# Optimization experiments

Measured on AMD Instinct MI355X. Metric: run time of the kernel, lower is better.

Reference implementation:

```python
import jax, jax.numpy as jnp
import numpy as np
import math

NUM_HEADS = 32
KV_CHANNELS = 128
LAYER_NUMBER = 4
# apply_query_key_layer_scaling=True: norm_factor = sqrt(head_dim) * layer_number,
# then scores are re-multiplied by layer_number in fp32 (numerics trick).
NORM_FACTOR = math.sqrt(KV_CHANNELS) * LAYER_NUMBER
COEFF = float(LAYER_NUMBER)
NEG = -1e9


def setup_inputs() -> dict:
    key = jax.random.key(0)
    k1, k2, k3 = jax.random.split(key, 3)
    b, h, s, d = 2, NUM_HEADS, 2048, KV_CHANNELS
    q = jax.random.normal(k1, (b, h, s, d), dtype=jnp.float32)
    k = jax.random.normal(k2, (b, h, s, d), dtype=jnp.float32)
    v = jax.random.normal(k3, (b, h, s, d), dtype=jnp.float32)
    # additive causal mask: 0 where allowed (j <= i), large negative where masked
    causal = jnp.tril(jnp.ones((s, s), dtype=bool))
    mask = jnp.where(causal, 0.0, NEG).astype(jnp.float32)[None, None, :, :]
    mask = jnp.broadcast_to(mask, (b, 1, s, s))
    return {"query_layer": q, "key_layer": k, "value_layer": v, "attention_mask": mask}


def reference(query_layer, key_layer, value_layer, attention_mask):
    b, h, sq, d = query_layer.shape
    skv = key_layer.shape[2]
    # baddbmm with beta=0, alpha=1/norm_factor  ==  (Q K^T) / norm_factor
    scores = jnp.einsum('bhqd,bhkd->bhqk', query_layer, key_layer) / NORM_FACTOR
    # attention_softmax_in_fp32 + layer scaling coefficient
    scores = scores.astype(jnp.float32) * COEFF
    scores = scores + attention_mask[:, :, :, :skv]
    probs = jax.nn.softmax(scores, axis=-1).astype(value_layer.dtype)
    # dropout p=0.0 -> identity
    context = jnp.einsum('bhqk,bhkd->bhqd', probs, value_layer)
    # transpose to [b, sq, h, d] then merge heads -> [b, sq, h*d]
    context = context.transpose(0, 2, 1, 3).reshape(b, sq, h * d)
    return context
```

## Files before the change

### kernel.cpp

```cpp
#include <hip/hip_runtime.h>
#include <cstdint>
#include <cstddef>

typedef __attribute__((ext_vector_type(8))) __bf16 bf16x8;
typedef __attribute__((ext_vector_type(4))) __bf16 bf16x4;
typedef __attribute__((ext_vector_type(4))) short s16x4;
typedef __attribute__((ext_vector_type(4))) float f32x4;
typedef __attribute__((ext_vector_type(2))) float f32x2;

#define SEQ 2048
#define DIM 128
#define NHEAD 32
#define NBATCH 2
#define NHEADS_TOTAL (NHEAD * NBATCH)
#define QSC (0.08838834764831845f * 1.4426950408889634f)

#define KV_TILE 32
#define TILES_PER_HEAD (SEQ / KV_TILE)
#define TILE_ELEMS (KV_TILE * DIM)
#define K_WS_BYTES ((size_t)NHEADS_TOTAL * TILES_PER_HEAD * TILE_ELEMS * 2)
#define WS_NEEDED (2 * K_WS_BYTES)

#define PS 40

__device__ __forceinline__ float fexp2(float x) {
#if __has_builtin(__builtin_amdgcn_exp2f)
  return __builtin_amdgcn_exp2f(x);
#else
  return __expf(x * 0.69314718055994531f);
#endif
}

__device__ __forceinline__ f32x4 mfma16(bf16x4 a, bf16x4 b, f32x4 c) {
#if __has_builtin(__builtin_amdgcn_mfma_f32_16x16x16_bf16)
  return __builtin_amdgcn_mfma_f32_16x16x16_bf16(a, b, c, 0, 0, 0);
#else
  return __builtin_amdgcn_mfma_f32_16x16x16bf16_1k(
      __builtin_bit_cast(s16x4, a), __builtin_bit_cast(s16x4, b), c, 0, 0, 0);
#endif
}

__device__ __forceinline__ void tile_barrier() {
  __builtin_amdgcn_sched_barrier(0);
  asm volatile("s_waitcnt lgkmcnt(0)" ::: "memory");
  __builtin_amdgcn_sched_barrier(0);
  __builtin_amdgcn_s_barrier();
  __builtin_amdgcn_sched_barrier(0);
}

__global__ __launch_bounds__(256) void glm_prepass(const float* __restrict__ Kg,
                                                   const float* __restrict__ Vg,
                                                   __bf16* __restrict__ Kws,
                                                   __bf16* __restrict__ Vws) {
  __shared__ float Vl[32 * 132];
  const int hd = blockIdx.x >> 6;
  const int t  = blockIdx.x & 63;
  const int i  = threadIdx.x;
  const int kv = i >> 3, seg = i & 7;
  const size_t src   = ((size_t)hd * SEQ + (size_t)t * 32 + kv) * DIM + seg * 16;
  const size_t tbase = (size_t)(hd * TILES_PER_HEAD + t) * TILE_ELEMS;

  {
    f32x4 a = *(const f32x4*)(Kg + src);
    f32x4 b = *(const f32x4*)(Kg + src + 4);
    f32x4 c4 = *(const f32x4*)(Kg + src + 8);
    f32x4 d4 = *(const f32x4*)(Kg + src + 12);
    bf16x8 A, B;
#pragma unroll
    for (int j = 0; j < 4; ++j) {
      A[j] = (__bf16)a[j]; A[4 + j] = (__bf16)b[j];
      B[j] = (__bf16)c4[j]; B[4 + j] = (__bf16)d4[j];
    }
    const int cf = kv >> 4, lc = kv & 15, cc = seg >> 1, q0 = (seg & 1) * 2;
    const int chunkA = (cf * 4 + cc) * 64 + q0 * 16 + lc;
    *(bf16x8*)&Kws[tbase + (size_t)chunkA * 8] = A;
    *(bf16x8*)&Kws[tbase + (size_t)(chunkA + 16) * 8] = B;
  }

  {
    f32x4 a = *(const f32x4*)(Vg + src);
    f32x4 b = *(const f32x4*)(Vg + src + 4);
    f32x4 c4 = *(const f32x4*)(Vg + src + 8);
    f32x4 d4 = *(const f32x4*)(Vg + src + 12);
    float* vl = &Vl[kv * 132 + seg * 16];
    *(f32x4*)(vl + 0) = a; *(f32x4*)(vl + 4) = b;
    *(f32x4*)(vl + 8) = c4; *(f32x4*)(vl + 12) = d4;
  }
  __syncthreads();
#pragma unroll
  for (int u = 0; u < 2; ++u) {
    const int ch = i * 2 + u;
    const int nt = ch >> 6, kvg = (ch >> 4) & 3, dd = ch & 15;
    bf16x8 wv;
#pragma unroll
    for (int e = 0; e < 8; ++e) wv[e] = (__bf16)Vl[(kvg * 8 + e) * 132 + nt * 16 + dd];
    *(bf16x8*)&Vws[tbase + (size_t)ch * 8] = wv;
  }
}

__global__ __launch_bounds__(256, 3) void glm_attn_main(const float* __restrict__ Qg,
                                                        const __bf16* __restrict__ Kws,
                                                        const __bf16* __restrict__ Vws,
                                                        float* __restrict__ Out) {
  __shared__ __align__(16) __bf16 Kb[2][TILE_ELEMS];
  __shared__ __align__(16) __bf16 Vb[2][TILE_ELEMS];

  const int tid  = threadIdx.x;
  const int w    = tid >> 6;
  const int lane = tid & 63;
  const int quad = lane >> 4;
  const int lcol = lane & 15;

  const int lin  = (int)blockIdx.x + ((int)blockIdx.y << 3) + ((int)blockIdx.z << 8);
  const int xcd  = lin & 7;
  const int k    = lin >> 3;
  const int head = xcd + ((k >> 3) << 3);
  const int pair = k & 7;
  const int hi   = head & 31, bi = head >> 5;
  const int hd   = bi * NHEAD + hi;

  const float*  Qh   = Qg + (size_t)hd * SEQ * DIM;
  const __bf16* Ksrc = Kws + (size_t)hd * TILES_PER_HEAD * TILE_ELEMS;
  const __bf16* Vsrc = Vws + (size_t)hd * TILES_PER_HEAD * TILE_ELEMS;

  bf16x8 kst0, kst1, vst0, vst1;

#define PREFETCH_REGS(tt)                                                   \
  {                                                                         \
    const __bf16* ks = Ksrc + (size_t)(tt) * TILE_ELEMS + (size_t)tid * 8;  \
    const __bf16* vs = Vsrc + (size_t)(tt) * TILE_ELEMS + (size_t)tid * 8;  \
    kst0 = *(const bf16x8*)ks;    kst1 = *(const bf16x8*)(ks + 2048);       \
    vst0 = *(const bf16x8*)vs;    vst1 = *(const bf16x8*)(vs + 2048);       \
  }

#define WRITE_LDS(b)                                                        \
  {                                                                         \
    *(bf16x8*)&Kb[b][tid * 8]        = kst0;                                \
    *(bf16x8*)&Kb[b][tid * 8 + 2048] = kst1;                                \
    *(bf16x8*)&Vb[b][tid * 8]        = vst0;                                \
    *(bf16x8*)&Vb[b][tid * 8 + 2048] = vst1;                                \
  }

  const int vofs0 = ((quad >> 1)) * 128 + lcol * 8 + (quad & 1) * 4;
  const int vofs1 = (2 + (quad >> 1)) * 128 + lcol * 8 + (quad & 1) * 4;

  for (int band = 0; band < 2; ++band) {
    const int qx = band ? (15 - pair) : pair;
    const int qb = qx * 128;
    const int T = qx * 4 + 4;
    const int Tfull = qx * 4;

    PREFETCH_REGS(0);

    bf16x8 qf[2][4];
#pragma unroll
    for (int m = 0; m < 2; ++m) {
      const float* qp = Qh + (size_t)(qb + w * 32 + m * 16 + lcol) * DIM + quad * 8;
#pragma unroll
      for (int cc = 0; cc < 4; ++cc) {
        f32x4 a = *(const f32x4*)(qp + cc * 32);
        f32x4 b = *(const f32x4*)(qp + cc * 32 + 4);
        bf16x8 t;
#pragma unroll
        for (int j = 0; j < 4; ++j) {
          t[j] = (__bf16)(a[j] * QSC);
          t[4 + j] = (__bf16)(b[j] * QSC);
        }
        qf[m][cc] = t;
      }
    }

    f32x4 o[2][8];
#pragma unroll
    for (int m = 0; m < 2; ++m)
#pragma unroll
      for (int n = 0; n < 8; ++n) o[m][n] = f32x4{0.f, 0.f, 0.f, 0.f};
    float lsum[2] = {0.0f, 0.0f};

    tile_barrier();
    WRITE_LDS(0);
    PREFETCH_REGS(1);

    for (int t = 0; t < T; ++t) {
      const int cur = t & 1;
      tile_barrier();

      const __bf16* Kc = Kb[cur];
      const __bf16* Vc = Vb[cur];

      f32x4 s2[2][2];
      s2[0][0] = s2[0][1] = s2[1][0] = s2[1][1] = f32x4{0.f, 0.f, 0.f, 0.f};
#pragma unroll
      for (int cc = 0; cc < 4; ++cc) {
        bf16x8 k0 = *(const bf16x8*)&Kc[cc * 512 + lane * 8];
        bf16x8 k1 = *(const bf16x8*)&Kc[(4 + cc) * 512 + lane * 8];
        s2[0][0] = __builtin_amdgcn_mfma_f32_16x16x32_bf16(k0, qf[0][cc], s2[0][0], 0, 0, 0);
        s2[0][1] = __builtin_amdgcn_mfma_f32_16x16x32_bf16(k0, qf[1][cc], s2[0][1], 0, 0, 0);
        s2[1][0] = __builtin_amdgcn_mfma_f32_16x16x32_bf16(k1, qf[0][cc], s2[1][0], 0, 0, 0);
        s2[1][1] = __builtin_amdgcn_mfma_f32_16x16x32_bf16(k1, qf[1][cc], s2[1][1], 0, 0, 0);
      }

      if (t + 1 < T) {
        if (cur) WRITE_LDS(0) else WRITE_LDS(1)
        if (t + 2 < T) PREFETCH_REGS(t + 2);
      }

      bf16x4 pb[2][2];
#pragma unroll
      for (int m = 0; m < 2; ++m) {
        float pv[2][4];
        if (t < Tfull) {
#pragma unroll
          for (int cf = 0; cf < 2; ++cf)
#pragma unroll
            for (int rr = 0; rr < 4; ++rr)
              pv[cf][rr] = fexp2(fminf(s2[cf][m][rr], 30.0f));
        } else {
          const int qg = qb + w * 32 + m * 16 + lcol;
          const int kv0 = t * 32 + quad * 4;
#pragma unroll
          for (int cf = 0; cf < 2; ++cf)
#pragma unroll
            for (int rr = 0; rr < 4; ++rr) {
              const int kvg = kv0 + cf * 16 + rr;
              pv[cf][rr] = (kvg <= qg) ? fexp2(fminf(s2[cf][m][rr], 30.0f)) : 0.0f;
            }
        }
#pragma unroll
        for (int cf = 0; cf < 2; ++cf) {
          lsum[m] += pv[cf][0] + pv[cf][1] + pv[cf][2] + pv[cf][3];
          bf16x4 pc;
#pragma unroll
          for (int rr = 0; rr < 4; ++rr) pc[rr] = (__bf16)pv[cf][rr];
          pb[m][cf] = pc;
        }
      }

#pragma unroll
      for (int nt = 0; nt < 8; ++nt) {
        bf16x4 v0 = *(const bf16x4*)&Vc[nt * 512 + vofs0];
        bf16x4 v1 = *(const bf16x4*)&Vc[nt * 512 + vofs1];
        o[0][nt] = mfma16(v0, pb[0][0], o[0][nt]);
        o[0][nt] = mfma16(v1, pb[0][1], o[0][nt]);
        o[1][nt] = mfma16(v0, pb[1][0], o[1][nt]);
        o[1][nt] = mfma16(v1, pb[1][1], o[1][nt]);
      }
    }

#pragma unroll
    for (int m = 0; m < 2; ++m) {
      float v = lsum[m];
      v += __shfl_xor(v, 16);
      v += __shfl_xor(v, 32);
      const float inv = 1.0f / v;
      const int q = qb + w * 32 + m * 16 + lcol;
      float* op = Out + ((size_t)bi * SEQ + q) * (NHEAD * DIM) + hi * DIM + quad * 4;
#pragma unroll
      for (int nt = 0; nt < 8; ++nt) {
        f32x4 st;
        st[0] = o[m][nt][0] * inv;
        st[1] = o[m][nt][1] * inv;
        st[2] = o[m][nt][2] * inv;
        st[3] = o[m][nt][3] * inv;
        *(f32x4*)(op + nt * 16) = st;
      }
    }
  }
}

__global__ __launch_bounds__(256, 2) void glm_attn_fused(
    const float* __restrict__ Qg, const float* __restrict__ Kg,
    const float* __restrict__ Vg, float* __restrict__ Out) {
  __shared__ __align__(16) __bf16 Kb[32 * DIM];
  __shared__ __align__(16) __bf16 Vb[32 * DIM];
  __shared__ __align__(16) __bf16 Pt[4][32 * PS];

  const int tid  = threadIdx.x;
  const int w    = tid >> 6;
  const int lane = tid & 63;
  const int quad = lane >> 4;
  const int lcol = lane & 15;

  const int qx = (int)gridDim.x - 1 - (int)blockIdx.x;
  const int qb = qx * 128;
  const int hi = blockIdx.y, bi = blockIdx.z;
  const int hd = bi * NHEAD + hi;

  const float* Qh = Qg + (size_t)hd * SEQ * DIM;
  const float* Kh = Kg + (size_t)hd * SEQ * DIM;
  const float* Vh = Vg + (size_t)hd * SEQ * DIM;

  const float* kbase = Kh + (size_t)lcol * DIM + w * 32 + quad * 8;
  const int vnt = tid >> 5, vkvg = (tid >> 3) & 3, vdd = (tid & 7) * 2;
  const float* vbase = Vh + (size_t)(vkvg * 8) * DIM + vnt * 16 + vdd;

  f32x4 kr0, kr1, kr2, kr3;
  f32x2 vr0, vr1, vr2, vr3, vr4, vr5, vr6, vr7;

#define PREFETCH_F(tt)                                                \
  {                                                                   \
    const float* ka = kbase + (size_t)(tt) * (32 * DIM);              \
    kr0 = *(const f32x4*)(ka);                                        \
    kr1 = *(const f32x4*)(ka + 4);                                    \
    kr2 = *(const f32x4*)(ka + 16 * DIM);                             \
    kr3 = *(const f32x4*)(ka + 16 * DIM + 4);                         \
    const float* va = vbase + (size_t)(tt) * (32 * DIM);              \
    vr0 = *(const f32x2*)(va + 0 * DIM);                              \
    vr1 = *(const f32x2*)(va + 1 * DIM);                              \
    vr2 = *(const f32x2*)(va + 2 * DIM);                              \
    vr3 = *(const f32x2*)(va + 3 * DIM);                              \
    vr4 = *(const f32x2*)(va + 4 * DIM);                              \
    vr5 = *(const f32x2*)(va + 5 * DIM);                              \
    vr6 = *(const f32x2*)(va + 6 * DIM);                              \
    vr7 = *(const f32x2*)(va + 7 * DIM);                              \
  }

  PREFETCH_F(0);

  bf16x8 qf[2][4];
#pragma unroll
  for (int m = 0; m < 2; ++m) {
    const float* qp = Qh + (size_t)(qb + w * 32 + m * 16 + lcol) * DIM + quad * 8;
#pragma unroll
    for (int c = 0; c < 4; ++c) {
      f32x4 a = *(const f32x4*)(qp + c * 32);
      f32x4 b = *(const f32x4*)(qp + c * 32 + 4);
      bf16x8 tq;
#pragma unroll
      for (int j = 0; j < 4; ++j) {
        tq[j] = (__bf16)(a[j] * QSC);
        tq[4 + j] = (__bf16)(b[j] * QSC);
      }
      qf[m][c] = tq;
    }
  }

  f32x4 o[2][8];
#pragma unroll
  for (int m = 0; m < 2; ++m)
#pragma unroll
    for (int n = 0; n < 8; ++n) o[m][n] = f32x4{0.f, 0.f, 0.f, 0.f};
  float lsum[2][4];
#pragma unroll
  for (int m = 0; m < 2; ++m)
#pragma unroll
    for (int r = 0; r < 4; ++r) lsum[m][r] = 0.0f;

  const int T = qx * 4 + 4;
  const int Tfull = qx * 4;

  for (int t = 0; t < T; ++t) {
    __syncthreads();
    {
      bf16x8 sA, sB;
#pragma unroll
      for (int j = 0; j < 4; ++j) {
        sA[j] = (__bf16)kr0[j]; sA[4 + j] = (__bf16)kr1[j];
        sB[j] = (__bf16)kr2[j]; sB[4 + j] = (__bf16)kr3[j];
      }
      *(bf16x8*)&Kb[tid * 8]        = sA;
      *(bf16x8*)&Kb[tid * 8 + 2048] = sB;
      bf16x8 v0, v1;
      v0[0] = (__bf16)vr0[0]; v1[0] = (__bf16)vr0[1];
      v0[1] = (__bf16)vr1[0]; v1[1] = (__bf16)vr1[1];
      v0[2] = (__bf16)vr2[0]; v1[2] = (__bf16)vr2[1];
      v0[3] = (__bf16)vr3[0]; v1[3] = (__bf16)vr3[1];
      v0[4] = (__bf16)vr4[0]; v1[4] = (__bf16)vr4[1];
      v0[5] = (__bf16)vr5[0]; v1[5] = (__bf16)vr5[1];
      v0[6] = (__bf16)vr6[0]; v1[6] = (__bf16)vr6[1];
      v0[7] = (__bf16)vr7[0]; v1[7] = (__bf16)vr7[1];
      *(bf16x8*)&Vb[tid * 16]     = v0;
      *(bf16x8*)&Vb[tid * 16 + 8] = v1;
    }
    __syncthreads();
    if (t + 1 < T) PREFETCH_F(t + 1);

    f32x4 s[2][2];
    s[0][0] = s[0][1] = s[1][0] = s[1][1] = f32x4{0.f, 0.f, 0.f, 0.f};
#pragma unroll
    for (int c = 0; c < 4; ++c) {
      bf16x8 k0 = *(const bf16x8*)&Kb[c * 512 + lane * 8];
      bf16x8 k1 = *(const bf16x8*)&Kb[(4 + c) * 512 + lane * 8];
      s[0][0] = __builtin_amdgcn_mfma_f32_16x16x32_bf16(qf[0][c], k0, s[0][0], 0, 0, 0);
      s[1][0] = __builtin_amdgcn_mfma_f32_16x16x32_bf16(qf[1][c], k0, s[1][0], 0, 0, 0);
      s[0][1] = __builtin_amdgcn_mfma_f32_16x16x32_bf16(qf[0][c], k1, s[0][1], 0, 0, 0);
      s[1][1] = __builtin_amdgcn_mfma_f32_16x16x32_bf16(qf[1][c], k1, s[1][1], 0, 0, 0);
    }

    __bf16* pw = Pt[w];
    if (t < Tfull) {
#pragma unroll
      for (int m = 0; m < 2; ++m)
#pragma unroll
        for (int cf = 0; cf < 2; ++cf)
#pragma unroll
          for (int r = 0; r < 4; ++r) {
            const float p = fexp2(fminf(s[m][cf][r], 30.0f));
            lsum[m][r] += p;
            pw[(m * 16 + quad * 4 + r) * PS + cf * 16 + lcol] = (__bf16)p;
          }
    } else {
      const int kvb = t * 32;
#pragma unroll
      for (int m = 0; m < 2; ++m) {
        const int rowb = qb + w * 32 + m * 16 + quad * 4;
#pragma unroll
        for (int cf = 0; cf < 2; ++cf) {
          const int col = kvb + cf * 16 + lcol;
#pragma unroll
          for (int r = 0; r < 4; ++r) {
            const float p = (col <= rowb + r) ? fexp2(fminf(s[m][cf][r], 30.0f)) : 0.0f;
            lsum[m][r] += p;
            pw[(m * 16 + quad * 4 + r) * PS + cf * 16 + lcol] = (__bf16)p;
          }
        }
      }
    }

    bf16x8 pf0 = *(const bf16x8*)&pw[lcol * PS + quad * 8];
    bf16x8 pf1 = *(const bf16x8*)&pw[(16 + lcol) * PS + quad * 8];
#pragma unroll
    for (int nt = 0; nt < 8; ++nt) {
      bf16x8 vf = *(const bf16x8*)&Vb[nt * 512 + lane * 8];
      o[0][nt] = __builtin_amdgcn_mfma_f32_16x16x32_bf16(pf0, vf, o[0][nt], 0, 0, 0);
      o[1][nt] = __builtin_amdgcn_mfma_f32_16x16x32_bf16(pf1, vf, o[1][nt], 0, 0, 0);
    }
  }

#pragma unroll
  for (int m = 0; m < 2; ++m)
#pragma unroll
    for (int r = 0; r < 4; ++r) {
      float v = lsum[m][r];
      v += __shfl_xor(v, 1); v += __shfl_xor(v, 2);
      v += __shfl_xor(v, 4); v += __shfl_xor(v, 8);
      lsum[m][r] = 1.0f / v;
    }
#pragma unroll
  for (int m = 0; m < 2; ++m) {
    const int row0 = qb + w * 32 + m * 16 + quad * 4;
#pragma unroll
    for (int r = 0; r < 4; ++r) {
      const float inv = lsum[m][r];
      float* op = Out + ((size_t)bi * SEQ + row0 + r) * (NHEAD * DIM) + hi * DIM + lcol;
#pragma unroll
      for (int nt = 0; nt < 8; ++nt) op[nt * 16] = o[m][nt][r] * inv;
    }
  }
}

extern "C" void kernel_launch(void* const* d_in, const int* in_sizes, int n_in,
                              void* d_out, int out_size, void* d_ws, size_t ws_size,
                              hipStream_t stream) {
  const float* Q = (const float*)d_in[0];
  const float* K = (const float*)d_in[1];
  const float* V = (const float*)d_in[2];
  float* Out = (float*)d_out;

  if (ws_size >= WS_NEEDED) {
    __bf16* Kws = (__bf16*)d_ws;
    __bf16* Vws = (__bf16*)((char*)d_ws + K_WS_BYTES);
    glm_prepass<<<dim3(NHEADS_TOTAL * TILES_PER_HEAD), 256, 0, stream>>>(K, V, Kws, Vws);
    glm_attn_main<<<dim3(8, NHEAD, NBATCH), 256, 0, stream>>>(Q, Kws, Vws, Out);
  } else {
    glm_attn_fused<<<dim3(SEQ / 128, NHEAD, NBATCH), 256, 0, stream>>>(Q, K, V, Out);
  }
}
```

Baseline: 326.1 us.

## Halve query tile to 64 rows per block and double grid size

Shrinks the main attention kernel's query band from 128 to 64 rows, so each wave handles 16 query rows instead of 32, and doubles the grid to 16x32x2 blocks while still pairing bands for causal load balance. Per-thread accumulators drop by half and launch bounds rise to 4 blocks per CU, aiming for more parallelism and occupancy. The cost is that each K/V tile loaded into LDS now serves half as many queries, which doubles K/V global and LDS traffic per unit of work.

```diff
diff --git a/kernel.cpp b/kernel.cpp
--- a/kernel.cpp
+++ b/kernel.cpp
@@ -98,7 +98,7 @@
   }
 }
 
-__global__ __launch_bounds__(256, 3) void glm_attn_main(const float* __restrict__ Qg,
+__global__ __launch_bounds__(256, 4) void glm_attn_main(const float* __restrict__ Qg,
                                                         const __bf16* __restrict__ Kws,
                                                         const __bf16* __restrict__ Vws,
                                                         float* __restrict__ Out) {
@@ -111,11 +111,11 @@
   const int quad = lane >> 4;
   const int lcol = lane & 15;
 
-  const int lin  = (int)blockIdx.x + ((int)blockIdx.y << 3) + ((int)blockIdx.z << 8);
+  const int lin  = (int)blockIdx.x + ((int)blockIdx.y << 4) + ((int)blockIdx.z << 9);
   const int xcd  = lin & 7;
   const int k    = lin >> 3;
-  const int head = xcd + ((k >> 3) << 3);
-  const int pair = k & 7;
+  const int head = xcd + ((k >> 4) << 3);
+  const int pair = k & 15;
   const int hi   = head & 31, bi = head >> 5;
   const int hd   = bi * NHEAD + hi;
 
@@ -145,17 +145,16 @@
   const int vofs1 = (2 + (quad >> 1)) * 128 + lcol * 8 + (quad & 1) * 4;
 
   for (int band = 0; band < 2; ++band) {
-    const int qx = band ? (15 - pair) : pair;
-    const int qb = qx * 128;
-    const int T = qx * 4 + 4;
-    const int Tfull = qx * 4;
+    const int qx = band ? (31 - pair) : pair;
+    const int qb = qx * 64;
+    const int T = qx * 2 + 2;
+    const int Tfull = qx * 2;
 
     PREFETCH_REGS(0);
 
-    bf16x8 qf[2][4];
-#pragma unroll
-    for (int m = 0; m < 2; ++m) {
-      const float* qp = Qh + (size_t)(qb + w * 32 + m * 16 + lcol) * DIM + quad * 8;
+    bf16x8 qf[4];
+    {
+      const float* qp = Qh + (size_t)(qb + w * 16 + lcol) * DIM + quad * 8;
 #pragma unroll
       for (int cc = 0; cc < 4; ++cc) {
         f32x4 a = *(const f32x4*)(qp + cc * 32);
@@ -166,16 +165,14 @@
           t[j] = (__bf16)(a[j] * QSC);
           t[4 + j] = (__bf16)(b[j] * QSC);
         }
-        qf[m][cc] = t;
-      }
-    }
-
-    f32x4 o[2][8];
-#pragma unroll
-    for (int m = 0; m < 2; ++m)
-#pragma unroll
-      for (int n = 0; n < 8; ++n) o[m][n] = f32x4{0.f, 0.f, 0.f, 0.f};
-    float lsum[2] = {0.0f, 0.0f};
+        qf[cc] = t;
+      }
+    }
+
+    f32x4 o[8];
+#pragma unroll
+    for (int n = 0; n < 8; ++n) o[n] = f32x4{0.f, 0.f, 0.f, 0.f};
+    float lsum = 0.0f;
 
     tile_barrier();
     WRITE_LDS(0);
@@ -188,16 +185,14 @@
       const __bf16* Kc = Kb[cur];
       const __bf16* Vc = Vb[cur];
 
-      f32x4 s2[2][2];
-      s2[0][0] = s2[0][1] = s2[1][0] = s2[1][1] = f32x4{0.f, 0.f, 0.f, 0.f};
+      f32x4 s2[2];
+      s2[0] = s2[1] = f32x4{0.f, 0.f, 0.f, 0.f};
 #pragma unroll
       for (int cc = 0; cc < 4; ++cc) {
         bf16x8 k0 = *(const bf16x8*)&Kc[cc * 512 + lane * 8];
         bf16x8 k1 = *(const bf16x8*)&Kc[(4 + cc) * 512 + lane * 8];
-        s2[0][0] = __builtin_amdgcn_mfma_f32_16x16x32_bf16(k0, qf[0][cc], s2[0][0], 0, 0, 0);
-        s2[0][1] = __builtin_amdgcn_mfma_f32_16x16x32_bf16(k0, qf[1][cc], s2[0][1], 0, 0, 0);
-        s2[1][0] = __builtin_amdgcn_mfma_f32_16x16x32_bf16(k1, qf[0][cc], s2[1][0], 0, 0, 0);
-        s2[1][1] = __builtin_amdgcn_mfma_f32_16x16x32_bf16(k1, qf[1][cc], s2[1][1], 0, 0, 0);
+        s2[0] = __builtin_amdgcn_mfma_f32_16x16x32_bf16(k0, qf[cc], s2[0], 0, 0, 0);
+        s2[1] = __builtin_amdgcn_mfma_f32_16x16x32_bf16(k1, qf[cc], s2[1], 0, 0, 0);
       }
 
       if (t + 1 < T) {
@@ -205,34 +200,33 @@
         if (t + 2 < T) PREFETCH_REGS(t + 2);
       }
 
-      bf16x4 pb[2][2];
-#pragma unroll
-      for (int m = 0; m < 2; ++m) {
+      bf16x4 pb[2];
+      {
         float pv[2][4];
         if (t < Tfull) {
 #pragma unroll
           for (int cf = 0; cf < 2; ++cf)
 #pragma unroll
             for (int rr = 0; rr < 4; ++rr)
-              pv[cf][rr] = fexp2(fminf(s2[cf][m][rr], 30.0f));
+              pv[cf][rr] = fexp2(fminf(s2[cf][rr], 30.0f));
         } else {
-          const int qg = qb + w * 32 + m * 16 + lcol;
+          const int qg = qb + w * 16 + lcol;
           const int kv0 = t * 32 + quad * 4;
 #pragma unroll
           for (int cf = 0; cf < 2; ++cf)
 #pragma unroll
             for (int rr = 0; rr < 4; ++rr) {
               const int kvg = kv0 + cf * 16 + rr;
-              pv[cf][rr] = (kvg <= qg) ? fexp2(fminf(s2[cf][m][rr], 30.0f)) : 0.0f;
+              pv[cf][rr] = (kvg <= qg) ? fexp2(fminf(s2[cf][rr], 30.0f)) : 0.0f;
             }
         }
 #pragma unroll
         for (int cf = 0; cf < 2; ++cf) {
-          lsum[m] += pv[cf][0] + pv[cf][1] + pv[cf][2] + pv[cf][3];
+          lsum += pv[cf][0] + pv[cf][1] + pv[cf][2] + pv[cf][3];
           bf16x4 pc;
 #pragma unroll
           for (int rr = 0; rr < 4; ++rr) pc[rr] = (__bf16)pv[cf][rr];
-          pb[m][cf] = pc;
+          pb[cf] = pc;
         }
       }
 
@@ -240,28 +234,25 @@
       for (int nt = 0; nt < 8; ++nt) {
         bf16x4 v0 = *(const bf16x4*)&Vc[nt * 512 + vofs0];
         bf16x4 v1 = *(const bf16x4*)&Vc[nt * 512 + vofs1];
-        o[0][nt] = mfma16(v0, pb[0][0], o[0][nt]);
-        o[0][nt] = mfma16(v1, pb[0][1], o[0][nt]);
-        o[1][nt] = mfma16(v0, pb[1][0], o[1][nt]);
-        o[1][nt] = mfma16(v1, pb[1][1], o[1][nt]);
-      }
-    }
-
-#pragma unroll
-    for (int m = 0; m < 2; ++m) {
-      float v = lsum[m];
+        o[nt] = mfma16(v0, pb[0], o[nt]);
+        o[nt] = mfma16(v1, pb[1], o[nt]);
+      }
+    }
+
+    {
+      float v = lsum;
       v += __shfl_xor(v, 16);
       v += __shfl_xor(v, 32);
       const float inv = 1.0f / v;
-      const int q = qb + w * 32 + m * 16 + lcol;
+      const int q = qb + w * 16 + lcol;
       float* op = Out + ((size_t)bi * SEQ + q) * (NHEAD * DIM) + hi * DIM + quad * 4;
 #pragma unroll
       for (int nt = 0; nt < 8; ++nt) {
         f32x4 st;
-        st[0] = o[m][nt][0] * inv;
-        st[1] = o[m][nt][1] * inv;
-        st[2] = o[m][nt][2] * inv;
-        st[3] = o[m][nt][3] * inv;
+        st[0] = o[nt][0] * inv;
+        st[1] = o[nt][1] * inv;
+        st[2] = o[nt][2] * inv;
+        st[3] = o[nt][3] * inv;
         *(f32x4*)(op + nt * 16) = st;
       }
     }
@@ -461,7 +452,7 @@
     __bf16* Kws = (__bf16*)d_ws;
     __bf16* Vws = (__bf16*)((char*)d_ws + K_WS_BYTES);
     glm_prepass<<<dim3(NHEADS_TOTAL * TILES_PER_HEAD), 256, 0, stream>>>(K, V, Kws, Vws);
-    glm_attn_main<<<dim3(8, NHEAD, NBATCH), 256, 0, stream>>>(Q, Kws, Vws, Out);
+    glm_attn_main<<<dim3(16, NHEAD, NBATCH), 256, 0, stream>>>(Q, Kws, Vws, Out);
   } else {
     glm_attn_fused<<<dim3(SEQ / 128, NHEAD, NBATCH), 256, 0, stream>>>(Q, K, V, Out);
   }
```

New measurement: 328.7 us. Within noise of the previous version (+0.8%).
